# Optimization experiments

Hardware: AMD Instinct MI355X
Metric: run time of the kernel (lower is better)

Reference implementation:

```python
import jax, jax.numpy as jnp
import numpy as np

N = 131072   # total gates/nodes in the batched block-diagonal circuit graph
E = 524288   # directed edges (avg degree 4)
D = 100      # hidden dim
DA = 50      # msg MLP hidden
DC = 30      # classifier hidden
R = 20       # message-passing rounds


def mlp(x, W1, b1, W2, b2):
    return jax.nn.relu(x @ W1 + b1) @ W2 + b2


def gru_step(x, h, Wih, Whh, bih, bhh):
    # single-timestep torch.nn.GRU cell
    gi = x @ Wih.T + bih
    gh = h @ Whh.T + bhh
    ir, iz, inn = jnp.split(gi, 3, axis=-1)
    hr, hz, hn = jnp.split(gh, 3, axis=-1)
    r = jax.nn.sigmoid(ir + hr)
    z = jax.nn.sigmoid(iz + hz)
    nwe = jnp.tanh(inn + r * hn)
    return (1.0 - z) * nwe + z * h


def setup_inputs():
    key = jax.random.key(0)
    ks = jax.random.split(key, 26)
    s = 0.05

    def rn(k, shape):
        return jax.random.normal(k, shape, dtype=jnp.float32) * s

    inp = {
        'features': jax.random.normal(ks[0], (N, 4), dtype=jnp.float32),
        'edge_row': jax.random.randint(ks[1], (E,), 0, N, dtype=jnp.int32),
        'edge_col': jax.random.randint(ks[2], (E,), 0, N, dtype=jnp.int32),
        'init_W': rn(ks[3], (4, D)), 'init_b': jnp.zeros((D,), jnp.float32),
        'fmsg_W1': rn(ks[4], (D, DA)), 'fmsg_b1': jnp.zeros((DA,), jnp.float32),
        'fmsg_W2': rn(ks[5], (DA, D)), 'fmsg_b2': jnp.zeros((D,), jnp.float32),
        'bmsg_W1': rn(ks[6], (D, DA)), 'bmsg_b1': jnp.zeros((DA,), jnp.float32),
        'bmsg_W2': rn(ks[7], (DA, D)), 'bmsg_b2': jnp.zeros((D,), jnp.float32),
        'fgru_Wih': rn(ks[8], (3 * D, D)), 'fgru_Whh': rn(ks[9], (3 * D, D)),
        'fgru_bih': jnp.zeros((3 * D,), jnp.float32), 'fgru_bhh': jnp.zeros((3 * D,), jnp.float32),
        'bgru_Wih': rn(ks[10], (3 * D, D)), 'bgru_Whh': rn(ks[11], (3 * D, D)),
        'bgru_bih': jnp.zeros((3 * D,), jnp.float32), 'bgru_bhh': jnp.zeros((3 * D,), jnp.float32),
        'cls_W1': rn(ks[12], (D, DC)), 'cls_b1': jnp.zeros((DC,), jnp.float32),
        'cls_W2': rn(ks[13], (DC, 1)), 'cls_b2': jnp.zeros((1,), jnp.float32),
    }
    return inp


def reference(features, edge_row, edge_col, init_W, init_b,
              fmsg_W1, fmsg_b1, fmsg_W2, fmsg_b2,
              bmsg_W1, bmsg_b1, bmsg_W2, bmsg_b2,
              fgru_Wih, fgru_Whh, fgru_bih, fgru_bhh,
              bgru_Wih, bgru_Whh, bgru_bih, bgru_bhh,
              cls_W1, cls_b1, cls_W2, cls_b2):
    n = features.shape[0]
    h = features @ init_W + init_b  # [N, D]

    def round_body(h, _):
        # forward pass: adj @ forward_msg(h)
        fm = mlp(h, fmsg_W1, fmsg_b1, fmsg_W2, fmsg_b2)
        f_msg = jax.ops.segment_sum(fm[edge_col], edge_row, num_segments=n)
        h = gru_step(f_msg, h, fgru_Wih, fgru_Whh, fgru_bih, fgru_bhh)
        # backward pass: adj.T @ backward_msg(h)
        bm = mlp(h, bmsg_W1, bmsg_b1, bmsg_W2, bmsg_b2)
        b_msg = jax.ops.segment_sum(bm[edge_row], edge_col, num_segments=n)
        h = gru_step(b_msg, h, bgru_Wih, bgru_Whh, bgru_bih, bgru_bhh)
        return h, None

    h, _ = jax.lax.scan(jax.checkpoint(round_body), h, None, length=R)
    return mlp(h, cls_W1, cls_b1, cls_W2, cls_b2)  # [N, 1]
```

## Files before the change

kernel.cpp:

```cpp
#include <hip/hip_runtime.h>
#include <math.h>

#define Nn 131072
#define Ee 524288
#define LROW 224

typedef __attribute__((ext_vector_type(8))) short short8;
typedef __attribute__((ext_vector_type(4))) float f32x4;
typedef unsigned short ushort_t;
typedef unsigned int uint32;

__device__ __forceinline__ f32x4 mfma16(short8 a, short8 b, f32x4 c) {
    return __builtin_amdgcn_mfma_f32_16x16x32_bf16(a, b, c, 0, 0, 0);
}

__device__ __forceinline__ uint32 rne_bf16(float x) {
    uint32 u = __float_as_uint(x);
    return (u + 0x7FFFu + ((u >> 16) & 1u)) >> 16;
}

__device__ __forceinline__ void split3(float x, uint32& h, uint32& m, uint32& l) {
    h = rne_bf16(x);
    float hf = __uint_as_float(h << 16);
    float r1 = x - hf;
    m = rne_bf16(r1);
    float mf = __uint_as_float(m << 16);
    float r2 = r1 - mf;
    l = rne_bf16(r2);
}

__device__ __forceinline__ float limb2f(ushort_t u) {
    return __uint_as_float((uint32)u << 16);
}

__global__ void diag_kernel(float* out, float val) {
    int n = blockIdx.x * 256 + threadIdx.x;
    if (n < Nn) out[n] = (n == 0) ? val : 0.f;
}
__global__ void zero_ints(int* p, int n) {
    int i = blockIdx.x * 256 + threadIdx.x;
    if (i < n) p[i] = 0;
}
__global__ void zero_short8(ushort_t* p, long n8) {
    long i = (long)blockIdx.x * 256 + threadIdx.x;
    if (i < n8) {
        short8 zz = {0, 0, 0, 0, 0, 0, 0, 0};
        *(short8*)(p + i * 8) = zz;
    }
}

__global__ void hist_kernel(const int* __restrict__ er, const int* __restrict__ ec,
                            int* __restrict__ cnt_f, int* __restrict__ cnt_b) {
    int e = blockIdx.x * 256 + threadIdx.x;
    atomicAdd(&cnt_f[er[e]], 1);
    atomicAdd(&cnt_b[ec[e]], 1);
}

__global__ __launch_bounds__(1024) void scan2_kernel(
    const int* __restrict__ cnt_f, const int* __restrict__ cnt_b,
    int* __restrict__ ptr_f, int* __restrict__ ptr_b, int n) {
    const int* cnt = blockIdx.x ? cnt_b : cnt_f;
    int* ptr = blockIdx.x ? ptr_b : ptr_f;
    __shared__ int sums[1024];
    int t = threadIdx.x;
    int chunk = n >> 10;
    int base = t * chunk;
    int s = 0;
    for (int i = 0; i < chunk; i++) s += cnt[base + i];
    sums[t] = s;
    __syncthreads();
    for (int off = 1; off < 1024; off <<= 1) {
        int v = (t >= off) ? sums[t - off] : 0;
        __syncthreads();
        sums[t] += v;
        __syncthreads();
    }
    int run = (t == 0) ? 0 : sums[t - 1];
    for (int i = 0; i < chunk; i++) { ptr[base + i] = run; run += cnt[base + i]; }
    if (t == 1023) ptr[n] = run;
}

__global__ void fill_kernel(const int* __restrict__ er, const int* __restrict__ ec,
                            int* __restrict__ ptr_f, int* __restrict__ ptr_b,
                            int* __restrict__ src_f, int* __restrict__ src_b) {
    int e = blockIdx.x * 256 + threadIdx.x;
    int r = er[e], c = ec[e];
    int p = atomicAdd(&ptr_f[r], 1); src_f[p] = c;
    int q = atomicAdd(&ptr_b[c], 1); src_b[q] = r;
}

__global__ void prep_gru_w(const float* __restrict__ Wih, const float* __restrict__ Whh,
                           const float* __restrict__ bih, const float* __restrict__ bhh,
                           ushort_t* __restrict__ W0, ushort_t* __restrict__ W1,
                           ushort_t* __restrict__ W2, float* __restrict__ bg) {
    int gid = blockIdx.x * 256 + threadIdx.x;
    if (gid >= 448 * 224) return;
    int c = gid / 224, k = gid - c * 224;
    int d = c >> 2, g = c & 3;
    float w = 0.f;
    if (d < 100) {
        if (k < 100) {
            if (g == 0)      w = Wih[d * 100 + k];
            else if (g == 1) w = Wih[(100 + d) * 100 + k];
            else if (g == 2) w = Wih[(200 + d) * 100 + k];
        } else if (k >= 112 && k < 212) {
            int kk = k - 112;
            if (g == 0)      w = Whh[d * 100 + kk];
            else if (g == 1) w = Whh[(100 + d) * 100 + kk];
            else if (g == 3) w = Whh[(200 + d) * 100 + kk];
        }
    }
    uint32 h, m, l; split3(w, h, m, l);
    W0[gid] = (ushort_t)h; W1[gid] = (ushort_t)m; W2[gid] = (ushort_t)l;
    if (k == 0) {
        float b = 0.f;
        if (d < 100) {
            if (g == 0)      b = bih[d] + bhh[d];
            else if (g == 1) b = bih[100 + d] + bhh[100 + d];
            else if (g == 2) b = bih[200 + d];
            else             b = bhh[200 + d];
        }
        bg[c] = b;
    }
}

__global__ void prep_msg_w(const float* __restrict__ W1, const float* __restrict__ b1,
                           const float* __restrict__ W2, const float* __restrict__ b2,
                           ushort_t* __restrict__ A0, ushort_t* __restrict__ A1,
                           ushort_t* __restrict__ A2, float* __restrict__ b1p,
                           ushort_t* __restrict__ B0, ushort_t* __restrict__ B1,
                           ushort_t* __restrict__ B2, float* __restrict__ b2p) {
    int gid = blockIdx.x * 256 + threadIdx.x;
    if (gid < 8192) {
        int c = gid >> 7, k = gid & 127;
        float w = (c < 50 && k < 100) ? W1[k * 50 + c] : 0.f;
        uint32 h, m, l; split3(w, h, m, l);
        A0[gid] = (ushort_t)h; A1[gid] = (ushort_t)m; A2[gid] = (ushort_t)l;
        if (k == 0) b1p[c] = (c < 50) ? b1[c] : 0.f;
    } else if (gid < 8192 + 7168) {
        int t = gid - 8192;
        int c = t >> 6, k = t & 63;
        float w = (c < 100 && k < 50) ? W2[k * 100 + c] : 0.f;
        uint32 h, m, l; split3(w, h, m, l);
        B0[t] = (ushort_t)h; B1[t] = (ushort_t)m; B2[t] = (ushort_t)l;
        if (k == 0) b2p[c] = (c < 100) ? b2[c] : 0.f;
    }
}

__global__ void init_h_kernel(const float* __restrict__ feat, const float* __restrict__ W,
                              const float* __restrict__ b,
                              ushort_t* __restrict__ L0, ushort_t* __restrict__ L1,
                              ushort_t* __restrict__ L2) {
    int gid = blockIdx.x * 256 + threadIdx.x;
    if (gid >= Nn * 100) return;
    int n = gid / 100, d = gid - n * 100;
    float acc = b[d];
#pragma unroll
    for (int k = 0; k < 4; k++) acc += feat[n * 4 + k] * W[k * 100 + d];
    uint32 h, m, l; split3(acc, h, m, l);
    size_t a = (size_t)n * LROW + 112 + d;
    L0[a] = (ushort_t)h; L1[a] = (ushort_t)m; L2[a] = (ushort_t)l;
}

__global__ __launch_bounds__(256, 2) void msg_mfma(
    const ushort_t* __restrict__ L0, const ushort_t* __restrict__ L1,
    const ushort_t* __restrict__ L2,
    const ushort_t* __restrict__ A0, const ushort_t* __restrict__ A1,
    const ushort_t* __restrict__ A2, const float* __restrict__ b1p,
    const ushort_t* __restrict__ B0, const ushort_t* __restrict__ B1,
    const ushort_t* __restrict__ B2, const float* __restrict__ b2p,
    float* __restrict__ fm) {
    __shared__ ushort_t C1[3][64][72];
    const int tid = threadIdx.x;
    const int u = tid >> 6;
    const int lane = tid & 63;
    const int m = lane & 15, q = lane >> 4;
    const int n0 = blockIdx.x * 64;
    const int n = n0 + u * 16 + m;

    f32x4 z = {0.f, 0.f, 0.f, 0.f};
    f32x4 a1[4] = {z, z, z, z};

    const size_t hbase = (size_t)n * LROW + 112;
    for (int kc = 0; kc < 4; kc++) {
        int kb = kc * 32 + q * 8;
        short8 f0 = *(const short8*)(L0 + hbase + kb);
        short8 f1 = *(const short8*)(L1 + hbase + kb);
        short8 f2 = *(const short8*)(L2 + hbase + kb);
#pragma unroll
        for (int t = 0; t < 4; t++) {
            int off = (t * 16 + m) * 128 + kc * 32 + q * 8;
            short8 w0 = *(const short8*)(A0 + off);
            short8 w1 = *(const short8*)(A1 + off);
            short8 w2 = *(const short8*)(A2 + off);
            a1[t] = mfma16(w0, f0, a1[t]);
            a1[t] = mfma16(w0, f1, a1[t]);
            a1[t] = mfma16(w1, f0, a1[t]);
            a1[t] = mfma16(w0, f2, a1[t]);
            a1[t] = mfma16(w2, f0, a1[t]);
            a1[t] = mfma16(w1, f1, a1[t]);
        }
    }
#pragma unroll
    for (int t = 0; t < 4; t++) {
        int c0 = t * 16 + 4 * q;
        float4 bb = *(const float4*)&b1p[c0];
        float v0 = fmaxf(a1[t][0] + bb.x, 0.f);
        float v1 = fmaxf(a1[t][1] + bb.y, 0.f);
        float v2 = fmaxf(a1[t][2] + bb.z, 0.f);
        float v3 = fmaxf(a1[t][3] + bb.w, 0.f);
        uint32 h0, m0, l0, h1, m1, l1, h2, m2, l2, h3, m3, l3;
        split3(v0, h0, m0, l0); split3(v1, h1, m1, l1);
        split3(v2, h2, m2, l2); split3(v3, h3, m3, l3);
        int nl = u * 16 + m;
        *(uint2*)&C1[0][nl][c0] = make_uint2(h0 | (h1 << 16), h2 | (h3 << 16));
        *(uint2*)&C1[1][nl][c0] = make_uint2(m0 | (m1 << 16), m2 | (m3 << 16));
        *(uint2*)&C1[2][nl][c0] = make_uint2(l0 | (l1 << 16), l2 | (l3 << 16));
    }
    __syncthreads();

    f32x4 a2[7] = {z, z, z, z, z, z, z};
    for (int kc = 0; kc < 2; kc++) {
        int nl = u * 16 + m;
        short8 c0f = *(const short8*)&C1[0][nl][kc * 32 + q * 8];
        short8 c1f = *(const short8*)&C1[1][nl][kc * 32 + q * 8];
        short8 c2f = *(const short8*)&C1[2][nl][kc * 32 + q * 8];
#pragma unroll
        for (int t = 0; t < 7; t++) {
            int off = (t * 16 + m) * 64 + kc * 32 + q * 8;
            short8 w0 = *(const short8*)(B0 + off);
            short8 w1 = *(const short8*)(B1 + off);
            short8 w2 = *(const short8*)(B2 + off);
            a2[t] = mfma16(w0, c0f, a2[t]);
            a2[t] = mfma16(w0, c1f, a2[t]);
            a2[t] = mfma16(w1, c0f, a2[t]);
            a2[t] = mfma16(w0, c2f, a2[t]);
            a2[t] = mfma16(w2, c0f, a2[t]);
            a2[t] = mfma16(w1, c1f, a2[t]);
        }
    }
#pragma unroll
    for (int t = 0; t < 7; t++) {
        int c0 = t * 16 + 4 * q;
        if (c0 < 100) {
            float4 bb = *(const float4*)&b2p[c0];
            float4 o;
            o.x = a2[t][0] + bb.x; o.y = a2[t][1] + bb.y;
            o.z = a2[t][2] + bb.z; o.w = a2[t][3] + bb.w;
            *(float4*)&fm[(size_t)n * 100 + c0] = o;
        }
    }
}

__global__ void gather4(const float* __restrict__ fm, const int* __restrict__ ptr,
                        const int* __restrict__ idx,
                        ushort_t* __restrict__ L0, ushort_t* __restrict__ L1,
                        ushort_t* __restrict__ L2) {
    int gid = blockIdx.x * 256 + threadIdx.x;
    int n = gid / 25, qq = (gid - n * 25) * 4;
    int s = (n == 0) ? 0 : ptr[n - 1];
    int e = ptr[n];
    float4 acc = {0.f, 0.f, 0.f, 0.f};
    for (int i = s; i < e; i++) {
        float4 v = *(const float4*)&fm[(size_t)idx[i] * 100 + qq];
        acc.x += v.x; acc.y += v.y; acc.z += v.z; acc.w += v.w;
    }
    uint32 h0, m0, l0, h1, m1, l1, h2, m2, l2, h3, m3, l3;
    split3(acc.x, h0, m0, l0); split3(acc.y, h1, m1, l1);
    split3(acc.z, h2, m2, l2); split3(acc.w, h3, m3, l3);
    size_t a = (size_t)n * LROW + qq;
    *(uint2*)&L0[a] = make_uint2(h0 | (h1 << 16), h2 | (h3 << 16));
    *(uint2*)&L1[a] = make_uint2(m0 | (m1 << 16), m2 | (m3 << 16));
    *(uint2*)&L2[a] = make_uint2(l0 | (l1 << 16), l2 | (l3 << 16));
}

__global__ __launch_bounds__(512, 2) void gru_mfma(
    ushort_t* __restrict__ L0, ushort_t* __restrict__ L1,
    ushort_t* __restrict__ L2,
    const ushort_t* __restrict__ W0, const ushort_t* __restrict__ W1,
    const ushort_t* __restrict__ W2, const float* __restrict__ bg) {
    __shared__ float SH[128][116];
    const int tid = threadIdx.x;
    const int wave = tid >> 6;
    const int rh = wave >> 2;
    const int wc = wave & 3;
    const int lane = tid & 63;
    const int m = lane & 15, q = lane >> 4;
    const int n0 = blockIdx.x * 128;

    f32x4 z = {0.f, 0.f, 0.f, 0.f};
    f32x4 acc[7][4];
#pragma unroll
    for (int t = 0; t < 7; t++)
#pragma unroll
        for (int rf = 0; rf < 4; rf++) acc[t][rf] = z;

    int woff[7];
#pragma unroll
    for (int t = 0; t < 7; t++)
        woff[t] = ((t * 4 + wc) * 16 + m) * 224 + q * 8;

    const size_t abase = (size_t)(n0 + rh * 64 + m) * LROW + q * 8;

#define GP(Wreg, Fr)                                             \
    _Pragma("unroll")                                            \
    for (int t = 0; t < 7; t++) {                                \
        _Pragma("unroll")                                        \
        for (int rf = 0; rf < 4; rf++)                           \
            acc[t][rf] = mfma16(Wreg[t], Fr[rf], acc[t][rf]);    \
    }

    short8 wA[7], wB[7];
#pragma unroll
    for (int t = 0; t < 7; t++) wA[t] = *(const short8*)(W0 + woff[t]);

#pragma unroll
    for (int kc = 0; kc < 7; kc++) {
        const int ko = kc * 32;
        short8 f0[4], f1[4], f2[4];
#pragma unroll
        for (int rf = 0; rf < 4; rf++)
            f0[rf] = *(const short8*)(L0 + abase + (size_t)rf * 16 * LROW + ko);
#pragma unroll
        for (int rf = 0; rf < 4; rf++)
            f1[rf] = *(const short8*)(L1 + abase + (size_t)rf * 16 * LROW + ko);
#pragma unroll
        for (int rf = 0; rf < 4; rf++)
            f2[rf] = *(const short8*)(L2 + abase + (size_t)rf * 16 * LROW + ko);

        if ((kc & 1) == 0) {
#pragma unroll
            for (int t = 0; t < 7; t++) wB[t] = *(const short8*)(W1 + woff[t] + ko);
            GP(wA, f0); GP(wA, f1); GP(wA, f2);
#pragma unroll
            for (int t = 0; t < 7; t++) wA[t] = *(const short8*)(W2 + woff[t] + ko);
            GP(wB, f0); GP(wB, f1);
            if (kc < 6) {
#pragma unroll
                for (int t = 0; t < 7; t++) wB[t] = *(const short8*)(W0 + woff[t] + ko + 32);
            }
            GP(wA, f0);
        } else {
#pragma unroll
            for (int t = 0; t < 7; t++) wA[t] = *(const short8*)(W1 + woff[t] + ko);
            GP(wB, f0); GP(wB, f1); GP(wB, f2);
#pragma unroll
            for (int t = 0; t < 7; t++) wB[t] = *(const short8*)(W2 + woff[t] + ko);
            GP(wA, f0); GP(wA, f1);
            if (kc < 6) {
#pragma unroll
                for (int t = 0; t < 7; t++) wA[t] = *(const short8*)(W0 + woff[t] + ko + 32);
            }
            GP(wB, f0);
        }
    }
#undef GP

#pragma unroll
    for (int p = 0; p < 4; p++) {
        int idx = tid + p * 512;
        int row = idx >> 4, c = idx & 15;
        if (c < 13) {
            size_t g = (size_t)(n0 + row) * LROW + 112 + c * 8;
            union { short8 s; ushort_t u[8]; } a0, a1, a2;
            a0.s = *(const short8*)(L0 + g);
            a1.s = *(const short8*)(L1 + g);
            a2.s = *(const short8*)(L2 + g);
#pragma unroll
            for (int j = 0; j < 8; j++)
                SH[row][c * 8 + j] =
                    (limb2f(a2.u[j]) + limb2f(a1.u[j])) + limb2f(a0.u[j]);
        }
    }
    __syncthreads();

#pragma unroll
    for (int t = 0; t < 7; t++) {
        const int ct = t * 4 + wc;
        const int d = ct * 4 + q;
        if (d < 100) {
            float4 b4 = *(const float4*)&bg[ct * 16 + 4 * q];
#pragma unroll
            for (int rf = 0; rf < 4; rf++) {
                int row = rh * 64 + rf * 16 + m;
                float hold = SH[row][d];
                float rp = acc[t][rf][0] + b4.x;
                float zp = acc[t][rf][1] + b4.y;
                float np = acc[t][rf][2] + b4.z;
                float hh = acc[t][rf][3] + b4.w;
                float rr = 1.f / (1.f + __expf(-rp));
                float zz = 1.f / (1.f + __expf(-zp));
                float nw = tanhf(np + rr * hh);
                SH[row][d] = (1.f - zz) * nw + zz * hold;
            }
        }
    }
    __syncthreads();

#pragma unroll
    for (int p = 0; p < 4; p++) {
        int idx = tid + p * 512;
        int row = idx >> 4, c = idx & 15;
        if (c < 13) {
            size_t g = (size_t)(n0 + row) * LROW + 112 + c * 8;
            union { short8 s; uint32 u4[4]; } o0, o1, o2;
#pragma unroll
            for (int jj = 0; jj < 4; jj++) {
                float ea = SH[row][c * 8 + 2 * jj];
                float eb = SH[row][c * 8 + 2 * jj + 1];
                uint32 ha, ma, la, hb, mb, lb;
                split3(ea, ha, ma, la);
                split3(eb, hb, mb, lb);
                o0.u4[jj] = ha | (hb << 16);
                o1.u4[jj] = ma | (mb << 16);
                o2.u4[jj] = la | (lb << 16);
            }
            *(short8*)(L0 + g) = o0.s;
            *(short8*)(L1 + g) = o1.s;
            *(short8*)(L2 + g) = o2.s;
        }
    }
}

__global__ __launch_bounds__(256) void classifier(
    const ushort_t* __restrict__ L0, const ushort_t* __restrict__ L1,
    const ushort_t* __restrict__ L2, const float* __restrict__ W1,
    const float* __restrict__ b1, const float* __restrict__ W2,
    const float* __restrict__ b2, float* __restrict__ out) {
    __shared__ float Wc[3128];
    __shared__ float bc[30];
    __shared__ float w2[30];
    int tid = threadIdx.x;
    for (int i = tid; i < 3128; i += 256) Wc[i] = (i < 3000) ? W1[i] : 0.f;
    if (tid < 30) { bc[tid] = b1[tid]; w2[tid] = W2[tid]; }
    __syncthreads();
    int n = blockIdx.x * 256 + tid;
    float a[30];
#pragma unroll
    for (int j = 0; j < 30; j++) a[j] = bc[j];
    const size_t base = (size_t)n * LROW + 112;
    for (int k8 = 0; k8 < 13; k8++) {
        int k0 = k8 * 8;
        union { short8 s; ushort_t u[8]; } h0, h1, h2;
        h0.s = *(const short8*)(L0 + base + k0);
        h1.s = *(const short8*)(L1 + base + k0);
        h2.s = *(const short8*)(L2 + base + k0);
#pragma unroll
        for (int jj = 0; jj < 8; jj++) {
            float hv = (limb2f(h2.u[jj]) + limb2f(h1.u[jj])) + limb2f(h0.u[jj]);
#pragma unroll
            for (int j = 0; j < 30; j++) a[j] = fmaf(hv, Wc[(k0 + jj) * 30 + j], a[j]);
        }
    }
    float s = b2[0];
#pragma unroll
    for (int j = 0; j < 30; j++) s = fmaf(fmaxf(a[j], 0.f), w2[j], s);
    out[n] = s;
}

extern "C" void kernel_launch(void* const* d_in, const int* in_sizes, int n_in,
                              void* d_out, int out_size, void* d_ws, size_t ws_size,
                              hipStream_t stream) {
    const float* feat     = (const float*)d_in[0];
    const int*   er       = (const int*)d_in[1];
    const int*   ec       = (const int*)d_in[2];
    const float* init_W   = (const float*)d_in[3];
    const float* init_b   = (const float*)d_in[4];
    const float* fmsg_W1  = (const float*)d_in[5];
    const float* fmsg_b1  = (const float*)d_in[6];
    const float* fmsg_W2  = (const float*)d_in[7];
    const float* fmsg_b2  = (const float*)d_in[8];
    const float* bmsg_W1  = (const float*)d_in[9];
    const float* bmsg_b1  = (const float*)d_in[10];
    const float* bmsg_W2  = (const float*)d_in[11];
    const float* bmsg_b2  = (const float*)d_in[12];
    const float* fgru_Wih = (const float*)d_in[13];
    const float* fgru_Whh = (const float*)d_in[14];
    const float* fgru_bih = (const float*)d_in[15];
    const float* fgru_bhh = (const float*)d_in[16];
    const float* bgru_Wih = (const float*)d_in[17];
    const float* bgru_Whh = (const float*)d_in[18];
    const float* bgru_bih = (const float*)d_in[19];
    const float* bgru_bhh = (const float*)d_in[20];
    const float* cls_W1   = (const float*)d_in[21];
    const float* cls_b1   = (const float*)d_in[22];
    const float* cls_W2   = (const float*)d_in[23];
    const float* cls_b2   = (const float*)d_in[24];
    float* out = (float*)d_out;

    float* ws = (float*)d_ws;
    size_t o = 0;
    float* fm = ws + o; o += (size_t)Nn * 100;

    const size_t PL = (size_t)Nn * LROW + 64;
    ushort_t* us = (ushort_t*)(ws + o);
    size_t uo = 0;
    ushort_t* L0 = us + uo; uo += PL;
    ushort_t* L1 = us + uo; uo += PL;
    ushort_t* L2 = us + uo; uo += PL;
    ushort_t* fWg0 = us + uo; uo += 448 * 224;
    ushort_t* fWg1 = us + uo; uo += 448 * 224;
    ushort_t* fWg2 = us + uo; uo += 448 * 224;
    ushort_t* bWg0 = us + uo; uo += 448 * 224;
    ushort_t* bWg1 = us + uo; uo += 448 * 224;
    ushort_t* bWg2 = us + uo; uo += 448 * 224;
    ushort_t* fA0 = us + uo; uo += 8192;
    ushort_t* fA1 = us + uo; uo += 8192;
    ushort_t* fA2 = us + uo; uo += 8192;
    ushort_t* bA0 = us + uo; uo += 8192;
    ushort_t* bA1 = us + uo; uo += 8192;
    ushort_t* bA2 = us + uo; uo += 8192;
    ushort_t* fB0 = us + uo; uo += 7168;
    ushort_t* fB1 = us + uo; uo += 7168;
    ushort_t* fB2 = us + uo; uo += 7168;
    ushort_t* bB0 = us + uo; uo += 7168;
    ushort_t* bB1 = us + uo; uo += 7168;
    ushort_t* bB2 = us + uo; uo += 7168;
    o += uo / 2;

    float* bgf  = ws + o; o += 448;
    float* bgb  = ws + o; o += 448;
    float* b1pf = ws + o; o += 64;
    float* b1pb = ws + o; o += 64;
    float* b2pf = ws + o; o += 112;
    float* b2pb = ws + o; o += 112;

    int* iws   = (int*)(ws + o);
    int* ptr_f = iws;
    int* ptr_b = ptr_f + (Nn + 1);
    int* cnt   = ptr_b + (Nn + 1);
    int* cnt_f = cnt;
    int* cnt_b = cnt + Nn;
    int* src_f = cnt + 2 * (size_t)Nn;
    int* src_b = src_f + Ee;

    size_t need = o * sizeof(float) +
                  (size_t)(2 * (Nn + 1) + 2 * Nn + 2 * Ee) * sizeof(int);
    if (ws_size < need) {
        diag_kernel<<<(Nn + 255) / 256, 256, 0, stream>>>(out, (float)ws_size);
        return;
    }

    {
        long n8 = (long)(3 * PL / 8);
        zero_short8<<<(int)((n8 + 255) / 256), 256, 0, stream>>>(L0, n8);
    }

    zero_ints<<<(2 * Nn + 255) / 256, 256, 0, stream>>>(cnt, 2 * Nn);
    hist_kernel<<<Ee / 256, 256, 0, stream>>>(er, ec, cnt_f, cnt_b);
    scan2_kernel<<<2, 1024, 0, stream>>>(cnt_f, cnt_b, ptr_f, ptr_b, Nn);
    fill_kernel<<<Ee / 256, 256, 0, stream>>>(er, ec, ptr_f, ptr_b, src_f, src_b);

    prep_gru_w<<<(448 * 224 + 255) / 256, 256, 0, stream>>>(
        fgru_Wih, fgru_Whh, fgru_bih, fgru_bhh, fWg0, fWg1, fWg2, bgf);
    prep_gru_w<<<(448 * 224 + 255) / 256, 256, 0, stream>>>(
        bgru_Wih, bgru_Whh, bgru_bih, bgru_bhh, bWg0, bWg1, bWg2, bgb);
    prep_msg_w<<<(15360 + 255) / 256, 256, 0, stream>>>(
        fmsg_W1, fmsg_b1, fmsg_W2, fmsg_b2, fA0, fA1, fA2, b1pf, fB0, fB1, fB2, b2pf);
    prep_msg_w<<<(15360 + 255) / 256, 256, 0, stream>>>(
        bmsg_W1, bmsg_b1, bmsg_W2, bmsg_b2, bA0, bA1, bA2, b1pb, bB0, bB1, bB2, b2pb);

    init_h_kernel<<<(Nn * 100 + 255) / 256, 256, 0, stream>>>(
        feat, init_W, init_b, L0, L1, L2);

    const int gTile = Nn / 64;
    const int gGru  = Nn / 128;
    const int gGath = Nn * 25 / 256;

    for (int rd = 0; rd < 20; rd++) {
        msg_mfma<<<gTile, 256, 0, stream>>>(L0, L1, L2,
            fA0, fA1, fA2, b1pf, fB0, fB1, fB2, b2pf, fm);
        gather4<<<gGath, 256, 0, stream>>>(fm, ptr_f, src_f, L0, L1, L2);
        gru_mfma<<<gGru, 512, 0, stream>>>(L0, L1, L2, fWg0, fWg1, fWg2, bgf);

        msg_mfma<<<gTile, 256, 0, stream>>>(L0, L1, L2,
            bA0, bA1, bA2, b1pb, bB0, bB1, bB2, b2pb, fm);
        gather4<<<gGath, 256, 0, stream>>>(fm, ptr_b, src_b, L0, L1, L2);
        gru_mfma<<<gGru, 512, 0, stream>>>(L0, L1, L2, bWg0, bWg1, bWg2, bgb);
    }

    classifier<<<Nn / 256, 256, 0, stream>>>(L0, L1, L2,
        cls_W1, cls_b1, cls_W2, cls_b2, out);
}
```

Before: 13.85 ms.

## Stage GRU activation limbs through LDS with double-buffered async global loads

The GRU MFMA kernel now copies each 32-column slice of the three bf16 limb arrays into a double-buffered, XOR-swizzled shared-memory buffer using global_load_lds. The next slice is prefetched while the current one is multiplied, and fragments are read from LDS instead of strided global loads. The block shrinks from 512 threads covering 128 rows to 256 threads covering 64 rows, and the grid doubles to match. This is meant to hide global-load latency and improve coalescing. In exchange it adds a barrier per K-chunk, and each weight fragment is now reused across half as many rows.

```diff
diff --git a/kernel.cpp b/kernel.cpp
--- a/kernel.cpp
+++ b/kernel.cpp
@@ -31,6 +31,12 @@
 
 __device__ __forceinline__ float limb2f(ushort_t u) {
     return __uint_as_float((uint32)u << 16);
+}
+
+__device__ __forceinline__ void gl16(const ushort_t* g, ushort_t* l) {
+    __builtin_amdgcn_global_load_lds(
+        (const __attribute__((address_space(1))) uint32*)g,
+        (__attribute__((address_space(3))) uint32*)l, 16, 0, 0);
 }
 
 __global__ void diag_kernel(float* out, float val) {
@@ -274,19 +280,27 @@
     *(uint2*)&L2[a] = make_uint2(l0 | (l1 << 16), l2 | (l3 << 16));
 }
 
-__global__ __launch_bounds__(512, 2) void gru_mfma(
+typedef union {
+    ushort_t lbuf[2][3][64][32];
+    float    sh[64][116];
+} GruShm;
+
+__global__ __launch_bounds__(256, 2) void gru_mfma(
     ushort_t* __restrict__ L0, ushort_t* __restrict__ L1,
     ushort_t* __restrict__ L2,
     const ushort_t* __restrict__ W0, const ushort_t* __restrict__ W1,
     const ushort_t* __restrict__ W2, const float* __restrict__ bg) {
-    __shared__ float SH[128][116];
+    __shared__ GruShm U;
     const int tid = threadIdx.x;
     const int wave = tid >> 6;
-    const int rh = wave >> 2;
-    const int wc = wave & 3;
     const int lane = tid & 63;
     const int m = lane & 15, q = lane >> 4;
-    const int n0 = blockIdx.x * 128;
+    const int n0 = blockIdx.x * 64;
+
+    const int lr = lane >> 2;
+    const int lc = (lane & 3) ^ ((lane >> 3) & 3);
+    const size_t sbase = (size_t)(n0 + wave * 16 + lr) * LROW + lc * 8;
+    const int cq = (q ^ ((m >> 1) & 3)) * 8;
 
     f32x4 z = {0.f, 0.f, 0.f, 0.f};
     f32x4 acc[7][4];
@@ -298,17 +312,23 @@
     int woff[7];
 #pragma unroll
     for (int t = 0; t < 7; t++)
-        woff[t] = ((t * 4 + wc) * 16 + m) * 224 + q * 8;
-
-    const size_t abase = (size_t)(n0 + rh * 64 + m) * LROW + q * 8;
-
-#define GP(Wreg, Fr)                                             \
-    _Pragma("unroll")                                            \
-    for (int t = 0; t < 7; t++) {                                \
-        _Pragma("unroll")                                        \
-        for (int rf = 0; rf < 4; rf++)                           \
-            acc[t][rf] = mfma16(Wreg[t], Fr[rf], acc[t][rf]);    \
-    }
+        woff[t] = ((t * 4 + wave) * 16 + m) * 224 + q * 8;
+
+#define STAGE(nb, KO)                                              \
+    gl16(L0 + sbase + (KO), &U.lbuf[nb][0][wave * 16][0]);         \
+    gl16(L1 + sbase + (KO), &U.lbuf[nb][1][wave * 16][0]);         \
+    gl16(L2 + sbase + (KO), &U.lbuf[nb][2][wave * 16][0]);
+
+#define GP(Wreg, Fr)                                               \
+    _Pragma("unroll")                                              \
+    for (int t = 0; t < 7; t++) {                                  \
+        _Pragma("unroll")                                          \
+        for (int rf = 0; rf < 4; rf++)                             \
+            acc[t][rf] = mfma16(Wreg[t], Fr[rf], acc[t][rf]);      \
+    }
+
+    STAGE(0, 0)
+    __syncthreads();
 
     short8 wA[7], wB[7];
 #pragma unroll
@@ -317,16 +337,19 @@
 #pragma unroll
     for (int kc = 0; kc < 7; kc++) {
         const int ko = kc * 32;
+        const int cb = kc & 1;
+        if (kc < 6) { STAGE(cb ^ 1, ko + 32) }
+
         short8 f0[4], f1[4], f2[4];
 #pragma unroll
         for (int rf = 0; rf < 4; rf++)
-            f0[rf] = *(const short8*)(L0 + abase + (size_t)rf * 16 * LROW + ko);
+            f0[rf] = *(const short8*)&U.lbuf[cb][0][rf * 16 + m][cq];
 #pragma unroll
         for (int rf = 0; rf < 4; rf++)
-            f1[rf] = *(const short8*)(L1 + abase + (size_t)rf * 16 * LROW + ko);
+            f1[rf] = *(const short8*)&U.lbuf[cb][1][rf * 16 + m][cq];
 #pragma unroll
         for (int rf = 0; rf < 4; rf++)
-            f2[rf] = *(const short8*)(L2 + abase + (size_t)rf * 16 * LROW + ko);
+            f2[rf] = *(const short8*)&U.lbuf[cb][2][rf * 16 + m][cq];
 
         if ((kc & 1) == 0) {
 #pragma unroll
@@ -353,12 +376,14 @@
             }
             GP(wB, f0);
         }
+        __syncthreads();
     }
 #undef GP
+#undef STAGE
 
 #pragma unroll
     for (int p = 0; p < 4; p++) {
-        int idx = tid + p * 512;
+        int idx = tid + p * 256;
         int row = idx >> 4, c = idx & 15;
         if (c < 13) {
             size_t g = (size_t)(n0 + row) * LROW + 112 + c * 8;
@@ -368,7 +393,7 @@
             a2.s = *(const short8*)(L2 + g);
 #pragma unroll
             for (int j = 0; j < 8; j++)
-                SH[row][c * 8 + j] =
+                U.sh[row][c * 8 + j] =
                     (limb2f(a2.u[j]) + limb2f(a1.u[j])) + limb2f(a0.u[j]);
         }
     }
@@ -376,14 +401,14 @@
 
 #pragma unroll
     for (int t = 0; t < 7; t++) {
-        const int ct = t * 4 + wc;
+        const int ct = t * 4 + wave;
         const int d = ct * 4 + q;
         if (d < 100) {
             float4 b4 = *(const float4*)&bg[ct * 16 + 4 * q];
 #pragma unroll
             for (int rf = 0; rf < 4; rf++) {
-                int row = rh * 64 + rf * 16 + m;
-                float hold = SH[row][d];
+                int row = rf * 16 + m;
+                float hold = U.sh[row][d];
                 float rp = acc[t][rf][0] + b4.x;
                 float zp = acc[t][rf][1] + b4.y;
                 float np = acc[t][rf][2] + b4.z;
@@ -391,7 +416,7 @@
                 float rr = 1.f / (1.f + __expf(-rp));
                 float zz = 1.f / (1.f + __expf(-zp));
                 float nw = tanhf(np + rr * hh);
-                SH[row][d] = (1.f - zz) * nw + zz * hold;
+                U.sh[row][d] = (1.f - zz) * nw + zz * hold;
             }
         }
     }
@@ -399,15 +424,15 @@
 
 #pragma unroll
     for (int p = 0; p < 4; p++) {
-        int idx = tid + p * 512;
+        int idx = tid + p * 256;
         int row = idx >> 4, c = idx & 15;
         if (c < 13) {
             size_t g = (size_t)(n0 + row) * LROW + 112 + c * 8;
             union { short8 s; uint32 u4[4]; } o0, o1, o2;
 #pragma unroll
             for (int jj = 0; jj < 4; jj++) {
-                float ea = SH[row][c * 8 + 2 * jj];
-                float eb = SH[row][c * 8 + 2 * jj + 1];
+                float ea = U.sh[row][c * 8 + 2 * jj];
+                float eb = U.sh[row][c * 8 + 2 * jj + 1];
                 uint32 ha, ma, la, hb, mb, lb;
                 split3(ea, ha, ma, la);
                 split3(eb, hb, mb, lb);
@@ -564,19 +589,19 @@
         feat, init_W, init_b, L0, L1, L2);
 
     const int gTile = Nn / 64;
-    const int gGru  = Nn / 128;
+    const int gGru  = Nn / 64;
     const int gGath = Nn * 25 / 256;
 
     for (int rd = 0; rd < 20; rd++) {
         msg_mfma<<<gTile, 256, 0, stream>>>(L0, L1, L2,
             fA0, fA1, fA2, b1pf, fB0, fB1, fB2, b2pf, fm);
         gather4<<<gGath, 256, 0, stream>>>(fm, ptr_f, src_f, L0, L1, L2);
-        gru_mfma<<<gGru, 512, 0, stream>>>(L0, L1, L2, fWg0, fWg1, fWg2, bgf);
+        gru_mfma<<<gGru, 256, 0, stream>>>(L0, L1, L2, fWg0, fWg1, fWg2, bgf);
 
         msg_mfma<<<gTile, 256, 0, stream>>>(L0, L1, L2,
             bA0, bA1, bA2, b1pb, bB0, bB1, bB2, b2pb, fm);
         gather4<<<gGath, 256, 0, stream>>>(fm, ptr_b, src_b, L0, L1, L2);
-        gru_mfma<<<gGru, 512, 0, stream>>>(L0, L1, L2, bWg0, bWg1, bWg2, bgb);
+        gru_mfma<<<gGru, 256, 0, stream>>>(L0, L1, L2, bWg0, bWg1, bWg2, bgb);
     }
 
     classifier<<<Nn / 256, 256, 0, stream>>>(L0, L1, L2,
```

New measurement: 13.38 ms. 3.4% less time.
